# Optimization experiments

Measured on AMD Instinct MI355X. Metric: run time of the kernel, lower is better.

The kernel has to match this reference:

```python
import jax, jax.numpy as jnp
import numpy as np

B_, S, D_IN, D_OUT, R = 4, 2048, 2048, 2048, 16

def setup_inputs() -> dict:
    key = jax.random.key(0)
    k = jax.random.split(key, 5)
    x = jax.random.normal(k[0], (B_, S, D_IN), dtype=jnp.float32)
    W = jax.random.normal(k[1], (D_OUT, D_IN), dtype=jnp.float32) * (1.0 / np.sqrt(D_IN))
    b = jax.random.normal(k[2], (D_OUT,), dtype=jnp.float32) * 0.02
    A = jax.random.normal(k[3], (R, D_IN), dtype=jnp.float32) * 0.02  # nn.init.normal_(std=0.02)
    Bm = jax.random.normal(k[4], (D_OUT, R), dtype=jnp.float32) * 0.02
    scale = jnp.asarray(0.8, dtype=jnp.float32)
    return {"x": x, "W": W, "b": b, "A": A, "B": Bm, "scale": scale}

def reference(x, W, b, A, B, scale):
    # base linear: y = x @ W^T + b
    orig = jnp.einsum('bsd,od->bso', x, W) + b
    # LoRA: scale * (x @ A^T) @ B^T
    h = jnp.einsum('bsd,rd->bsr', x, A)          # [B,S,r]
    lora = jnp.einsum('bsr,or->bso', h, B) * scale
    return orig + lora
```

## Files before the change

kernel.cpp:

```cpp
#include <hip/hip_runtime.h>
#include <hip/hip_bf16.h>
#include <cstdint>


typedef __bf16 bf16x8 __attribute__((ext_vector_type(8)));
typedef float floatx16 __attribute__((ext_vector_type(16)));
typedef unsigned short ushort8 __attribute__((ext_vector_type(8)));

#define BM 256
#define BN 256
#define BK 64
#define NT 32

__device__ __forceinline__ void gload_lds16(const void* g, void* l) {
    __builtin_amdgcn_global_load_lds((__attribute__((address_space(1))) void*)g,
                                     (__attribute__((address_space(3))) void*)l,
                                     16, 0, 0);
}

__device__ __forceinline__ unsigned short f2bf_bits(float f) {
    unsigned int u = __float_as_uint(f);
    u += 0x7FFFu + ((u >> 16) & 1u);
    return (unsigned short)(u >> 16);
}

__global__ __launch_bounds__(256)
void aux_kernel(const float* __restrict__ x, unsigned short* __restrict__ Xbf,
                const float* __restrict__ W, const float* __restrict__ A,
                const float* __restrict__ Bm, const float* __restrict__ scale_p,
                unsigned short* __restrict__ Weff)
{
    const int K = 2048, R = 16;
    int bid = blockIdx.x;
    if (bid < 8192) {
        size_t i = ((size_t)bid * 256 + threadIdx.x) * 8;
        float4 a = *reinterpret_cast<const float4*>(x + i);
        float4 b = *reinterpret_cast<const float4*>(x + i + 4);
        ushort8 o;
        o[0] = f2bf_bits(a.x); o[1] = f2bf_bits(a.y);
        o[2] = f2bf_bits(a.z); o[3] = f2bf_bits(a.w);
        o[4] = f2bf_bits(b.x); o[5] = f2bf_bits(b.y);
        o[6] = f2bf_bits(b.z); o[7] = f2bf_bits(b.w);
        *reinterpret_cast<ushort8*>(Xbf + i) = o;
    } else {
        int t  = (bid - 8192) * 256 + threadIdx.x;
        int n  = t >> 8;
        int k8 = (t & 255) << 3;

        float s = *scale_p;
        float br[16];
#pragma unroll
        for (int r = 0; r < R; ++r)
            br[r] = s * Bm[n * R + r];

        float acc[8] = {0,0,0,0,0,0,0,0};
#pragma unroll
        for (int r = 0; r < R; ++r) {
            const float* ap = A + r * K + k8;
#pragma unroll
            for (int j = 0; j < 8; ++j)
                acc[j] += br[r] * ap[j];
        }

        const float* wp = W + (size_t)n * K + k8;
        ushort8 o;
#pragma unroll
        for (int j = 0; j < 8; ++j)
            o[j] = f2bf_bits(wp[j] + acc[j]);
        *reinterpret_cast<ushort8*>(Weff + (size_t)n * K + k8) = o;
    }
}

#define BAR()       __builtin_amdgcn_s_barrier()
#define WAIT_LGKM() asm volatile("s_waitcnt lgkmcnt(0)" ::: "memory")
#define WAIT_VM4()  asm volatile("s_waitcnt vmcnt(4)" ::: "memory")
#define WAIT_VM0()  asm volatile("s_waitcnt vmcnt(0)" ::: "memory")

#define STAGE_A(buf, mh, kt) do {                                             \
    gload_lds16(gA0 + (size_t)(mh) * 64 * 2048 + (kt) * 64, &Sa[buf][mh][c0 * 8]); \
    gload_lds16(gA1 + (size_t)(mh) * 64 * 2048 + (kt) * 64, &Sa[buf][mh][c1 * 8]); \
} while (0)

#define STAGE_B(buf, nh, kt) do {                                             \
    gload_lds16(gB0 + (size_t)(nh) * 32 * 2048 + (kt) * 64, &Sb[buf][nh][c0 * 8]); \
    gload_lds16(gB1 + (size_t)(nh) * 32 * 2048 + (kt) * 64, &Sb[buf][nh][c1 * 8]); \
} while (0)

#define READ_A(buf, mh) do {                                                  \
    const unsigned short* ra = &Sa[buf][mh][(wr * 64 + l31) * 64];            \
    _Pragma("unroll")                                                         \
    for (int ks = 0; ks < 4; ++ks) {                                          \
        af[0][ks] = *reinterpret_cast<const bf16x8*>(ra + swzk[ks]);          \
        af[1][ks] = *reinterpret_cast<const bf16x8*>(ra + 2048 + swzk[ks]);   \
    }                                                                         \
} while (0)

#define READ_B(buf, nh, BQ) do {                                              \
    const unsigned short* rb = &Sb[buf][nh][(wc * 32 + l31) * 64];            \
    _Pragma("unroll")                                                         \
    for (int ks = 0; ks < 4; ++ks)                                            \
        BQ[ks] = *reinterpret_cast<const bf16x8*>(rb + swzk[ks]);             \
} while (0)

#define MFMAQ(mh, nh, BQ) do {                                                \
    __builtin_amdgcn_s_setprio(1);                                            \
    _Pragma("unroll")                                                         \
    for (int ks = 0; ks < 4; ++ks) {                                          \
        acc[(mh)*2+0][nh] = __builtin_amdgcn_mfma_f32_32x32x16_bf16(          \
            af[0][ks], BQ[ks], acc[(mh)*2+0][nh], 0, 0, 0);                   \
        acc[(mh)*2+1][nh] = __builtin_amdgcn_mfma_f32_32x32x16_bf16(          \
            af[1][ks], BQ[ks], acc[(mh)*2+1][nh], 0, 0, 0);                   \
    }                                                                         \
    __builtin_amdgcn_s_setprio(0);                                            \
} while (0)

__global__ __launch_bounds__(512)
void gemm_bias_kernel(const unsigned short* __restrict__ X,
                      const unsigned short* __restrict__ Wt,
                      const float* __restrict__ bias,
                      float* __restrict__ out)
{
    const int N = 2048, K = 2048;

    __shared__ alignas(16) unsigned short Sa[2][2][8192];
    __shared__ alignas(16) unsigned short Sb[2][2][8192];

    const int tid  = threadIdx.x;
    const int wave = tid >> 6;
    const int lane = tid & 63;
    const int l31  = lane & 31;
    const int kg   = lane >> 5;
    const int l7   = lane & 7;
    const int wr   = wave >> 2;
    const int wc   = wave & 3;

    const int id  = blockIdx.x;
    const int xcd = id & 7;
    const int sg  = id >> 3;
    const int bm  = (xcd * 4 + (sg & 3)) * BM;
    const int bn  = (sg >> 2) * BN;

    const int c0 = tid, c1 = tid + 512;
    const int ar0 = (c0 >> 3) & 63, as0 = c0 & 7;
    const int ar1 = (c1 >> 3) & 63, as1 = c1 & 7;
    const unsigned short* gA0 = X + (size_t)(bm + (c0 >> 9) * 128 + ar0) * K
                                  + ((as0 ^ (ar0 & 7) ^ ((ar0 >> 3) & 3)) << 3);
    const unsigned short* gA1 = X + (size_t)(bm + (c1 >> 9) * 128 + ar1) * K
                                  + ((as1 ^ (ar1 & 7) ^ ((ar1 >> 3) & 3)) << 3);
    const int br0 = (c0 >> 3) & 31, br1 = (c1 >> 3) & 31;
    const unsigned short* gB0 = Wt + (size_t)(bn + (c0 >> 8) * 64 + br0) * K
                                   + ((as0 ^ (br0 & 7) ^ ((br0 >> 3) & 3)) << 3);
    const unsigned short* gB1 = Wt + (size_t)(bn + (c1 >> 8) * 64 + br1) * K
                                   + ((as1 ^ (br1 & 7) ^ ((br1 >> 3) & 3)) << 3);

    const int fr   = l7 ^ (l31 >> 3);
    const int swzk[4] = { ((0 + kg) ^ fr) << 3, ((2 + kg) ^ fr) << 3,
                          ((4 + kg) ^ fr) << 3, ((6 + kg) ^ fr) << 3 };

    floatx16 acc[4][2] = {};
    bf16x8 af[2][4];
    bf16x8 bqa[4], bqb[4];

    STAGE_A(0, 0, 0);
    STAGE_B(0, 1, 0);
    STAGE_B(0, 0, 0);
    STAGE_A(0, 1, 0);
    STAGE_A(1, 0, 1);
    STAGE_B(1, 1, 1);
    WAIT_VM4(); BAR();

#pragma unroll 1
    for (int tt = 0; tt < NT; tt += 2) {
        const int t1 = tt + 1;
        const int t2 = (tt + 2 < NT) ? tt + 2 : NT - 1;
        const int t3 = (tt + 3 < NT) ? tt + 3 : NT - 1;

        READ_A(0, 0); READ_B(0, 0, bqa);
        STAGE_B(1, 0, t1);
        BAR(); WAIT_LGKM(); MFMAQ(0, 0, bqa); BAR();
        READ_B(0, 1, bqb);
        STAGE_A(1, 1, t1);
        BAR(); WAIT_LGKM(); MFMAQ(0, 1, bqb); BAR();
        READ_A(0, 1);
        STAGE_A(0, 0, t2);
        BAR(); WAIT_LGKM(); MFMAQ(1, 1, bqb); BAR();
        STAGE_B(0, 1, t2);
        BAR(); WAIT_LGKM(); MFMAQ(1, 0, bqa); WAIT_VM4(); BAR();

        READ_A(1, 0); READ_B(1, 0, bqa);
        STAGE_B(0, 0, t2);
        BAR(); WAIT_LGKM(); MFMAQ(0, 0, bqa); BAR();
        READ_B(1, 1, bqb);
        STAGE_A(0, 1, t2);
        BAR(); WAIT_LGKM(); MFMAQ(0, 1, bqb); BAR();
        READ_A(1, 1);
        STAGE_A(1, 0, t3);
        BAR(); WAIT_LGKM(); MFMAQ(1, 1, bqb); BAR();
        STAGE_B(1, 1, t3);
        BAR(); WAIT_LGKM(); MFMAQ(1, 0, bqa); WAIT_VM4(); BAR();
    }
    WAIT_VM0();

    const float bsv0 = bias[bn + wc * 64 + l31];
    const float bsv1 = bias[bn + wc * 64 + 32 + l31];
    const size_t cb  = (size_t)bn + wc * 64 + l31;
#pragma unroll
    for (int mb = 0; mb < 4; ++mb) {
#pragma unroll
        for (int r = 0; r < 16; ++r) {
            size_t rowoff = (size_t)(bm + wr * 128 + mb * 32
                                     + (r & 3) + ((r >> 2) << 3) + (kg << 2)) * N;
            out[rowoff + cb]      = acc[mb][0][r] + bsv0;
            out[rowoff + cb + 32] = acc[mb][1][r] + bsv1;
        }
    }
}

extern "C" void kernel_launch(void* const* d_in, const int* in_sizes, int n_in,
                              void* d_out, int out_size, void* d_ws, size_t ws_size,
                              hipStream_t stream)
{
    const float* x  = (const float*)d_in[0];
    const float* W  = (const float*)d_in[1];
    const float* b  = (const float*)d_in[2];
    const float* A  = (const float*)d_in[3];
    const float* Bm = (const float*)d_in[4];
    const float* sc = (const float*)d_in[5];
    float* out = (float*)d_out;

    const size_t M = 8192, N = 2048, K = 2048;

    unsigned short* Xbf  = (unsigned short*)d_ws;
    unsigned short* Weff = (unsigned short*)d_ws + M * K;

    aux_kernel<<<dim3((M * K + N * K) / 8 / 256), dim3(256), 0, stream>>>(
        x, Xbf, W, A, Bm, sc, Weff);

    gemm_bias_kernel<<<dim3((M / BM) * (N / BN)), dim3(512), 0, stream>>>(
        Xbf, Weff, b, out);
}
```

Before: 209.5 us.

## Fuse x fp32-to-bf16 conversion into GEMM A-tile staging via registers

Drops the separate pass that converts x to bf16 in workspace. The GEMM now loads fp32 x tiles into registers, converts them to bf16 and writes them swizzled into LDS, interleaved with the MFMA phases. This removes a full write and re-read of the bf16 copy of x. In exchange, each block reads twice as many bytes of x per tile, A no longer uses direct-to-LDS loads, and the extra conversion ALU work and register pressure (launch bounds set to 2) may slow the pipelined main loop.

```diff
diff --git a/kernel.cpp b/kernel.cpp
--- a/kernel.cpp
+++ b/kernel.cpp
@@ -25,65 +25,65 @@
 }
 
 __global__ __launch_bounds__(256)
-void aux_kernel(const float* __restrict__ x, unsigned short* __restrict__ Xbf,
-                const float* __restrict__ W, const float* __restrict__ A,
+void aux_kernel(const float* __restrict__ W, const float* __restrict__ A,
                 const float* __restrict__ Bm, const float* __restrict__ scale_p,
                 unsigned short* __restrict__ Weff)
 {
     const int K = 2048, R = 16;
-    int bid = blockIdx.x;
-    if (bid < 8192) {
-        size_t i = ((size_t)bid * 256 + threadIdx.x) * 8;
-        float4 a = *reinterpret_cast<const float4*>(x + i);
-        float4 b = *reinterpret_cast<const float4*>(x + i + 4);
-        ushort8 o;
-        o[0] = f2bf_bits(a.x); o[1] = f2bf_bits(a.y);
-        o[2] = f2bf_bits(a.z); o[3] = f2bf_bits(a.w);
-        o[4] = f2bf_bits(b.x); o[5] = f2bf_bits(b.y);
-        o[6] = f2bf_bits(b.z); o[7] = f2bf_bits(b.w);
-        *reinterpret_cast<ushort8*>(Xbf + i) = o;
-    } else {
-        int t  = (bid - 8192) * 256 + threadIdx.x;
-        int n  = t >> 8;
-        int k8 = (t & 255) << 3;
-
-        float s = *scale_p;
-        float br[16];
-#pragma unroll
-        for (int r = 0; r < R; ++r)
-            br[r] = s * Bm[n * R + r];
-
-        float acc[8] = {0,0,0,0,0,0,0,0};
-#pragma unroll
-        for (int r = 0; r < R; ++r) {
-            const float* ap = A + r * K + k8;
-#pragma unroll
-            for (int j = 0; j < 8; ++j)
-                acc[j] += br[r] * ap[j];
-        }
-
-        const float* wp = W + (size_t)n * K + k8;
-        ushort8 o;
+    int t  = blockIdx.x * 256 + threadIdx.x;
+    int n  = t >> 8;
+    int k8 = (t & 255) << 3;
+
+    float s = *scale_p;
+    float br[16];
+#pragma unroll
+    for (int r = 0; r < R; ++r)
+        br[r] = s * Bm[n * R + r];
+
+    float acc[8] = {0,0,0,0,0,0,0,0};
+#pragma unroll
+    for (int r = 0; r < R; ++r) {
+        const float* ap = A + r * K + k8;
 #pragma unroll
         for (int j = 0; j < 8; ++j)
-            o[j] = f2bf_bits(wp[j] + acc[j]);
-        *reinterpret_cast<ushort8*>(Weff + (size_t)n * K + k8) = o;
+            acc[j] += br[r] * ap[j];
     }
+
+    const float* wp = W + (size_t)n * K + k8;
+    ushort8 o;
+#pragma unroll
+    for (int j = 0; j < 8; ++j)
+        o[j] = f2bf_bits(wp[j] + acc[j]);
+    *reinterpret_cast<ushort8*>(Weff + (size_t)n * K + k8) = o;
 }
 
 #define BAR()       __builtin_amdgcn_s_barrier()
 #define WAIT_LGKM() asm volatile("s_waitcnt lgkmcnt(0)" ::: "memory")
-#define WAIT_VM4()  asm volatile("s_waitcnt vmcnt(4)" ::: "memory")
 #define WAIT_VM0()  asm volatile("s_waitcnt vmcnt(0)" ::: "memory")
-
-#define STAGE_A(buf, mh, kt) do {                                             \
-    gload_lds16(gA0 + (size_t)(mh) * 64 * 2048 + (kt) * 64, &Sa[buf][mh][c0 * 8]); \
-    gload_lds16(gA1 + (size_t)(mh) * 64 * 2048 + (kt) * 64, &Sa[buf][mh][c1 * 8]); \
-} while (0)
 
 #define STAGE_B(buf, nh, kt) do {                                             \
     gload_lds16(gB0 + (size_t)(nh) * 32 * 2048 + (kt) * 64, &Sb[buf][nh][c0 * 8]); \
     gload_lds16(gB1 + (size_t)(nh) * 32 * 2048 + (kt) * 64, &Sb[buf][nh][c1 * 8]); \
+} while (0)
+
+#define AISSUE_S(S, mh, kt) do {                                              \
+    const float* xp = xA + (size_t)(mh) * 64 * 2048 + (kt) * 64;              \
+    S[0] = *reinterpret_cast<const float4*>(xp);                              \
+    S[1] = *reinterpret_cast<const float4*>(xp + 4);                          \
+    S[2] = *reinterpret_cast<const float4*>(xp + 128 * 2048);                 \
+    S[3] = *reinterpret_cast<const float4*>(xp + 128 * 2048 + 4);             \
+} while (0)
+
+#define AWRITE_S(S, buf, mh) do {                                             \
+    ushort8 o0, o1;                                                           \
+    o0[0]=f2bf_bits(S[0].x); o0[1]=f2bf_bits(S[0].y); o0[2]=f2bf_bits(S[0].z);\
+    o0[3]=f2bf_bits(S[0].w); o0[4]=f2bf_bits(S[1].x); o0[5]=f2bf_bits(S[1].y);\
+    o0[6]=f2bf_bits(S[1].z); o0[7]=f2bf_bits(S[1].w);                         \
+    o1[0]=f2bf_bits(S[2].x); o1[1]=f2bf_bits(S[2].y); o1[2]=f2bf_bits(S[2].z);\
+    o1[3]=f2bf_bits(S[2].w); o1[4]=f2bf_bits(S[3].x); o1[5]=f2bf_bits(S[3].y);\
+    o1[6]=f2bf_bits(S[3].z); o1[7]=f2bf_bits(S[3].w);                         \
+    *reinterpret_cast<ushort8*>(&Sa[buf][mh][dstA])        = o0;              \
+    *reinterpret_cast<ushort8*>(&Sa[buf][mh][dstA + 4096]) = o1;              \
 } while (0)
 
 #define READ_A(buf, mh) do {                                                  \
@@ -114,8 +114,8 @@
     __builtin_amdgcn_s_setprio(0);                                            \
 } while (0)
 
-__global__ __launch_bounds__(512)
-void gemm_bias_kernel(const unsigned short* __restrict__ X,
+__global__ __launch_bounds__(512, 2)
+void gemm_bias_kernel(const float* __restrict__ x,
                       const unsigned short* __restrict__ Wt,
                       const float* __restrict__ bias,
                       float* __restrict__ out)
@@ -140,16 +140,18 @@
     const int bm  = (xcd * 4 + (sg & 3)) * BM;
     const int bn  = (sg >> 2) * BN;
 
+    const int ar = (tid >> 3) & 63;
+    const int as = tid & 7;
+    const float* xA = x + (size_t)(bm + ar) * K + as * 8;
+    const int dstA = ar * 64 + ((as ^ (ar & 7) ^ ((ar >> 3) & 3)) << 3);
+    float4 qA[4];
+    float4 qB[4];
+
     const int c0 = tid, c1 = tid + 512;
-    const int ar0 = (c0 >> 3) & 63, as0 = c0 & 7;
-    const int ar1 = (c1 >> 3) & 63, as1 = c1 & 7;
-    const unsigned short* gA0 = X + (size_t)(bm + (c0 >> 9) * 128 + ar0) * K
-                                  + ((as0 ^ (ar0 & 7) ^ ((ar0 >> 3) & 3)) << 3);
-    const unsigned short* gA1 = X + (size_t)(bm + (c1 >> 9) * 128 + ar1) * K
-                                  + ((as1 ^ (ar1 & 7) ^ ((ar1 >> 3) & 3)) << 3);
+    const int as1 = c1 & 7;
     const int br0 = (c0 >> 3) & 31, br1 = (c1 >> 3) & 31;
     const unsigned short* gB0 = Wt + (size_t)(bn + (c0 >> 8) * 64 + br0) * K
-                                   + ((as0 ^ (br0 & 7) ^ ((br0 >> 3) & 3)) << 3);
+                                   + ((as  ^ (br0 & 7) ^ ((br0 >> 3) & 3)) << 3);
     const unsigned short* gB1 = Wt + (size_t)(bn + (c1 >> 8) * 64 + br1) * K
                                    + ((as1 ^ (br1 & 7) ^ ((br1 >> 3) & 3)) << 3);
 
@@ -161,13 +163,14 @@
     bf16x8 af[2][4];
     bf16x8 bqa[4], bqb[4];
 
-    STAGE_A(0, 0, 0);
     STAGE_B(0, 1, 0);
     STAGE_B(0, 0, 0);
-    STAGE_A(0, 1, 0);
-    STAGE_A(1, 0, 1);
     STAGE_B(1, 1, 1);
-    WAIT_VM4(); BAR();
+    AISSUE_S(qB, 0, 0); AWRITE_S(qB, 0, 0);
+    AISSUE_S(qB, 1, 0); AWRITE_S(qB, 0, 1);
+    AISSUE_S(qB, 0, 1); AWRITE_S(qB, 1, 0);
+    AISSUE_S(qA, 1, 1);
+    WAIT_VM0(); WAIT_LGKM(); BAR();
 
 #pragma unroll 1
     for (int tt = 0; tt < NT; tt += 2) {
@@ -177,27 +180,31 @@
 
         READ_A(0, 0); READ_B(0, 0, bqa);
         STAGE_B(1, 0, t1);
+        AISSUE_S(qB, 0, t2);
         BAR(); WAIT_LGKM(); MFMAQ(0, 0, bqa); BAR();
+        AWRITE_S(qA, 1, 1);
         READ_B(0, 1, bqb);
-        STAGE_A(1, 1, t1);
         BAR(); WAIT_LGKM(); MFMAQ(0, 1, bqb); BAR();
+        AWRITE_S(qB, 0, 0);
         READ_A(0, 1);
-        STAGE_A(0, 0, t2);
         BAR(); WAIT_LGKM(); MFMAQ(1, 1, bqb); BAR();
         STAGE_B(0, 1, t2);
-        BAR(); WAIT_LGKM(); MFMAQ(1, 0, bqa); WAIT_VM4(); BAR();
+        AISSUE_S(qA, 1, t2);
+        BAR(); WAIT_LGKM(); MFMAQ(1, 0, bqa); BAR();
 
         READ_A(1, 0); READ_B(1, 0, bqa);
         STAGE_B(0, 0, t2);
+        AISSUE_S(qB, 0, t3);
         BAR(); WAIT_LGKM(); MFMAQ(0, 0, bqa); BAR();
+        AWRITE_S(qA, 0, 1);
         READ_B(1, 1, bqb);
-        STAGE_A(0, 1, t2);
         BAR(); WAIT_LGKM(); MFMAQ(0, 1, bqb); BAR();
+        AWRITE_S(qB, 1, 0);
         READ_A(1, 1);
-        STAGE_A(1, 0, t3);
         BAR(); WAIT_LGKM(); MFMAQ(1, 1, bqb); BAR();
         STAGE_B(1, 1, t3);
-        BAR(); WAIT_LGKM(); MFMAQ(1, 0, bqa); WAIT_VM4(); BAR();
+        AISSUE_S(qA, 1, t3);
+        BAR(); WAIT_LGKM(); MFMAQ(1, 0, bqa); BAR();
     }
     WAIT_VM0();
 
@@ -230,12 +237,11 @@
 
     const size_t M = 8192, N = 2048, K = 2048;
 
-    unsigned short* Xbf  = (unsigned short*)d_ws;
-    unsigned short* Weff = (unsigned short*)d_ws + M * K;
-
-    aux_kernel<<<dim3((M * K + N * K) / 8 / 256), dim3(256), 0, stream>>>(
-        x, Xbf, W, A, Bm, sc, Weff);
+    unsigned short* Weff = (unsigned short*)d_ws;
+
+    aux_kernel<<<dim3(N * K / 8 / 256), dim3(256), 0, stream>>>(
+        W, A, Bm, sc, Weff);
 
     gemm_bias_kernel<<<dim3((M / BM) * (N / BN)), dim3(512), 0, stream>>>(
-        Xbf, Weff, b, out);
-}
+        x, Weff, b, out);
+}
```

After: 258.1 us. +23.2%, slower.

## Merge GEMM main-loop quarter phases into half-tile phases with fewer barriers

Applied to the files above, without the earlier changes.

Restructures the double-buffered main loop so each phase reads both B halves and one A half, then issues 16 MFMAs covering both N halves. The number of barrier-separated phases per tile drops from four to two, and the prefetch order of LDS sub-buffers is changed to match. This cuts barrier and wait overhead and gives larger MFMA bursts. In exchange, fewer phases are left to hide the global-to-LDS loads, and register pressure rises because both B fragments are live at once.

```diff
diff --git a/kernel.cpp b/kernel.cpp
--- a/kernel.cpp
+++ b/kernel.cpp
@@ -102,14 +102,18 @@
         BQ[ks] = *reinterpret_cast<const bf16x8*>(rb + swzk[ks]);             \
 } while (0)
 
-#define MFMAQ(mh, nh, BQ) do {                                                \
+#define MFMAPH(mh) do {                                                       \
     __builtin_amdgcn_s_setprio(1);                                            \
     _Pragma("unroll")                                                         \
     for (int ks = 0; ks < 4; ++ks) {                                          \
-        acc[(mh)*2+0][nh] = __builtin_amdgcn_mfma_f32_32x32x16_bf16(          \
-            af[0][ks], BQ[ks], acc[(mh)*2+0][nh], 0, 0, 0);                   \
-        acc[(mh)*2+1][nh] = __builtin_amdgcn_mfma_f32_32x32x16_bf16(          \
-            af[1][ks], BQ[ks], acc[(mh)*2+1][nh], 0, 0, 0);                   \
+        acc[(mh)*2+0][0] = __builtin_amdgcn_mfma_f32_32x32x16_bf16(           \
+            af[0][ks], bqa[ks], acc[(mh)*2+0][0], 0, 0, 0);                   \
+        acc[(mh)*2+1][0] = __builtin_amdgcn_mfma_f32_32x32x16_bf16(           \
+            af[1][ks], bqa[ks], acc[(mh)*2+1][0], 0, 0, 0);                   \
+        acc[(mh)*2+0][1] = __builtin_amdgcn_mfma_f32_32x32x16_bf16(           \
+            af[0][ks], bqb[ks], acc[(mh)*2+0][1], 0, 0, 0);                   \
+        acc[(mh)*2+1][1] = __builtin_amdgcn_mfma_f32_32x32x16_bf16(           \
+            af[1][ks], bqb[ks], acc[(mh)*2+1][1], 0, 0, 0);                   \
     }                                                                         \
     __builtin_amdgcn_s_setprio(0);                                            \
 } while (0)
@@ -162,11 +166,11 @@
     bf16x8 bqa[4], bqb[4];
 
     STAGE_A(0, 0, 0);
+    STAGE_B(0, 0, 0);
     STAGE_B(0, 1, 0);
-    STAGE_B(0, 0, 0);
     STAGE_A(0, 1, 0);
     STAGE_A(1, 0, 1);
-    STAGE_B(1, 1, 1);
+    STAGE_B(1, 0, 1);
     WAIT_VM4(); BAR();
 
 #pragma unroll 1
@@ -175,29 +179,18 @@
         const int t2 = (tt + 2 < NT) ? tt + 2 : NT - 1;
         const int t3 = (tt + 3 < NT) ? tt + 3 : NT - 1;
 
-        READ_A(0, 0); READ_B(0, 0, bqa);
-        STAGE_B(1, 0, t1);
-        BAR(); WAIT_LGKM(); MFMAQ(0, 0, bqa); BAR();
-        READ_B(0, 1, bqb);
-        STAGE_A(1, 1, t1);
-        BAR(); WAIT_LGKM(); MFMAQ(0, 1, bqb); BAR();
+        READ_A(0, 0); READ_B(0, 0, bqa); READ_B(0, 1, bqb);
+        STAGE_A(1, 1, t1); STAGE_B(1, 1, t1);
+        BAR(); WAIT_LGKM(); MFMAPH(0); BAR();
         READ_A(0, 1);
-        STAGE_A(0, 0, t2);
-        BAR(); WAIT_LGKM(); MFMAQ(1, 1, bqb); BAR();
-        STAGE_B(0, 1, t2);
-        BAR(); WAIT_LGKM(); MFMAQ(1, 0, bqa); WAIT_VM4(); BAR();
-
-        READ_A(1, 0); READ_B(1, 0, bqa);
-        STAGE_B(0, 0, t2);
-        BAR(); WAIT_LGKM(); MFMAQ(0, 0, bqa); BAR();
-        READ_B(1, 1, bqb);
-        STAGE_A(0, 1, t2);
-        BAR(); WAIT_LGKM(); MFMAQ(0, 1, bqb); BAR();
+        STAGE_A(0, 0, t2); STAGE_B(0, 0, t2);
+        BAR(); WAIT_LGKM(); MFMAPH(1); WAIT_VM4(); BAR();
+        READ_A(1, 0); READ_B(1, 0, bqa); READ_B(1, 1, bqb);
+        STAGE_A(0, 1, t2); STAGE_B(0, 1, t2);
+        BAR(); WAIT_LGKM(); MFMAPH(0); BAR();
         READ_A(1, 1);
-        STAGE_A(1, 0, t3);
-        BAR(); WAIT_LGKM(); MFMAQ(1, 1, bqb); BAR();
-        STAGE_B(1, 1, t3);
-        BAR(); WAIT_LGKM(); MFMAQ(1, 0, bqa); WAIT_VM4(); BAR();
+        STAGE_A(1, 0, t3); STAGE_B(1, 0, t3);
+        BAR(); WAIT_LGKM(); MFMAPH(1); WAIT_VM4(); BAR();
     }
     WAIT_VM0();
 
```

Result: no change. 211.8 us (+1.1%).
